# Kernel optimization log

Measured on AMD Instinct MI355X. Metric: run time of the kernel, lower is better.

## Reference

```python
import jax, jax.numpy as jnp
import numpy as np

WEIGHT = 0.1  # init weight

# 6-connectivity (scipy generate_binary_structure(3,1)) neighbor reductions

def _nmin(x, fill):
    p = jnp.pad(x, 1, constant_values=fill)
    return jnp.minimum(
        jnp.minimum(jnp.minimum(p[:-2, 1:-1, 1:-1], p[2:, 1:-1, 1:-1]),
                    jnp.minimum(p[1:-1, :-2, 1:-1], p[1:-1, 2:, 1:-1])),
        jnp.minimum(p[1:-1, 1:-1, :-2], p[1:-1, 1:-1, 2:]))


def _nor(x):
    p = jnp.pad(x, 1, constant_values=False)
    return (p[:-2, 1:-1, 1:-1] | p[2:, 1:-1, 1:-1] |
            p[1:-1, :-2, 1:-1] | p[1:-1, 2:, 1:-1] |
            p[1:-1, 1:-1, :-2] | p[1:-1, 1:-1, 2:])


def _nand(x):
    # border_value=0 in scipy.binary_erosion -> pad with False
    p = jnp.pad(x, 1, constant_values=False)
    return (p[:-2, 1:-1, 1:-1] & p[2:, 1:-1, 1:-1] &
            p[1:-1, :-2, 1:-1] & p[1:-1, 2:, 1:-1] &
            p[1:-1, 1:-1, :-2] & p[1:-1, 1:-1, 2:])


def _cc_count(mask):
    # connected-component count via min-label propagation (6-connectivity),
    # equivalent to scipy.ndimage.label(...)[1]
    n = mask.size
    idx = jnp.arange(n, dtype=jnp.int32).reshape(mask.shape)
    big = jnp.int32(n)
    lbl0 = jnp.where(mask, idx, big)

    def body(c):
        lbl, _ = c
        new = jnp.where(mask, jnp.minimum(lbl, _nmin(lbl, big)), big)
        return new, jnp.any(new != lbl)

    lbl, _ = jax.lax.while_loop(lambda c: c[1], body, (lbl0, jnp.bool_(True)))
    # roots: voxels whose label equals their own index
    return jnp.sum(mask & (lbl == idx)).astype(jnp.int32)


def _cavity_volume(mask):
    # binary_fill_holes: background not reachable from the border
    bg = ~mask
    border = jnp.ones(mask.shape, bool).at[1:-1, 1:-1, 1:-1].set(False)
    r0 = bg & border

    def body(c):
        r, _ = c
        new = bg & (r | _nor(r))
        return new, jnp.any(new != r)

    reach, _ = jax.lax.while_loop(lambda c: c[1], body, (r0, jnp.bool_(True)))
    return jnp.sum(bg & ~reach).astype(jnp.int32)


def _betti(mask):
    b0 = _cc_count(mask)
    eroded = mask & _nand(mask)  # binary_erosion, iterations=1
    b0e = _cc_count(eroded)
    b1 = jnp.maximum(jnp.int32(0), b0 - b0e)
    b2 = _cavity_volume(mask) // 100
    return jnp.stack([b0, b1, b2]).astype(jnp.float32)


def setup_inputs() -> dict:
    key = jax.random.key(0)
    k1, k2 = jax.random.split(key)
    B, C, D, H, W = 2, 4, 64, 128, 128
    pred = jax.random.normal(k1, (B, C, D, H, W), dtype=jnp.float32)
    target = jax.random.randint(k2, (B, D, H, W), 0, C, dtype=jnp.int32)
    return {"pred": pred, "target": target}


def reference(pred, target):
    B, C = pred.shape[0], pred.shape[1]
    vol = pred.shape[2:]
    prob = jax.nn.softmax(pred, axis=1)
    # foreground classes 1..C-1, flattened to [B*(C-1), D, H, W]
    pred_masks = (prob[:, 1:] > 0.5).reshape((-1,) + vol)
    cls = jnp.arange(1, C, dtype=target.dtype).reshape(1, C - 1, 1, 1, 1)
    tgt_masks = (target[:, None] == cls).reshape((-1,) + vol)
    pb = jax.vmap(_betti)(pred_masks)  # [B*(C-1), 3]
    tb = jax.vmap(_betti)(tgt_masks)
    count = B * (C - 1)
    return WEIGHT * jnp.abs(pb - tb).sum() / count
```

## Files before the change

### kernel.cpp

```cpp
#include <hip/hip_runtime.h>
#include <stdint.h>

#define DD 64
#define HH 128
#define WW 128
#define NVOX (DD * HH * WW)
#define NWRD (NVOX / 32)
#define BATCH 2
#define NCLS 4
#define NMASK 12
#define NSLOT 24
#define NTILE 128
#define MAXC 2048
#define VNODE (NTILE * MAXC)
#define NODE_STRIDE (VNODE + 64)
#define NTASKW 7424
#define NTASKH (2 * NTASKW)

__device__ __forceinline__ int uf_find(int* P, int x) {
    while (true) {
        int p = P[x];
        if (p == x) return x;
        int gp = P[p];
        if (gp != p) P[x] = gp;
        x = gp;
    }
}
__device__ __forceinline__ int uf_find_ro(const int* P, int x) {
    int p;
    while ((p = P[x]) != x) x = p;
    return x;
}
__device__ __forceinline__ int2 uf_find2_ro(const int* P, int a, int b) {
    while (true) {
        int pa = P[a];
        int pb = P[b];
        bool da = (pa == a), db = (pb == b);
        if (da && db) return make_int2(a, b);
        a = pa; b = pb;
    }
}
__device__ __forceinline__ void uf_union(int* P, int a, int b) {
    while (true) {
        a = uf_find(P, a);
        b = uf_find(P, b);
        if (a == b) return;
        int lo = a < b ? a : b;
        int hi = a < b ? b : a;
        int old = atomicCAS(&P[hi], hi, lo);
        if (old == hi) return;
        a = lo; b = old;
    }
}

#define SW(v) ((v) + ((v) >> 5))
__device__ __forceinline__ int lfind(int* lp, int x) {
    while (true) {
        int p = lp[SW(x)];
        if (p == x) return x;
        int gp = lp[SW(p)];
        if (gp != p) lp[SW(x)] = gp;
        x = gp;
    }
}
__device__ __forceinline__ void lunion(int* lp, int a, int b) {
    while (true) {
        a = lfind(lp, a);
        b = lfind(lp, b);
        if (a == b) return;
        int lo = a < b ? a : b;
        int hi = a < b ? b : a;
        int old = atomicCAS(&lp[SW(hi)], hi, lo);
        if (old == hi) return;
        a = lo; b = old;
    }
}
__device__ __forceinline__ int lresolve(const int* lp, int h) {
    int v = lp[SW(h)];
    while (v >= 0) v = lp[SW(v)];
    return -v - 1;
}
__device__ __forceinline__ int run_head(uint32_t w, int p) {
    uint32_t below = ~w & ((1u << p) - 1u);
    return below ? (32 - __clz((int)below)) : 0;
}


__global__ void k_masks2(const float* __restrict__ pred, const int* __restrict__ tgt,
                         uint32_t* __restrict__ maskW, int* __restrict__ counts) {
    int tid = blockIdx.x * blockDim.x + threadIdx.x;
    if (tid < 64) counts[tid] = 0;
    int b = tid >> 20;
    int i = tid & (NVOX - 1);
    const float* p = pred + (size_t)b * NCLS * NVOX + i;
    float x0 = p[0], x1 = p[NVOX], x2 = p[2 * NVOX], x3 = p[3 * NVOX];
    float mx = fmaxf(fmaxf(x0, x1), fmaxf(x2, x3));
    float e0 = __expf(x0 - mx), e1 = __expf(x1 - mx), e2 = __expf(x2 - mx), e3 = __expf(x3 - mx);
    float S = e0 + e1 + e2 + e3;
    int t = tgt[(size_t)b * NVOX + i];
    int lane = threadIdx.x & 63;
    int wbase = i >> 5;
    float ev[3] = {e1, e2, e3};
    for (int c = 0; c < 3; ++c) {
        unsigned long long bal = __ballot(ev[c] / S > 0.5f);
        uint32_t* M = maskW + (size_t)(b * 3 + c) * NWRD;
        if (lane == 0)  M[wbase] = (uint32_t)bal;
        if (lane == 32) M[wbase] = (uint32_t)(bal >> 32);
        unsigned long long balT = __ballot(t == c + 1);
        uint32_t* MT = maskW + (size_t)(6 + b * 3 + c) * NWRD;
        if (lane == 0)  MT[wbase] = (uint32_t)balT;
        if (lane == 32) MT[wbase] = (uint32_t)(balT >> 32);
    }
}

__global__ void k_erode(const uint32_t* __restrict__ maskW, uint32_t* __restrict__ erodW) {
    int tid = blockIdx.x * blockDim.x + threadIdx.x;
    int m = tid / NWRD;
    int w = tid - m * NWRD;
    const uint32_t* M = maskW + (size_t)m * NWRD;
    int z = w >> 9, y = (w >> 2) & 127, q = w & 3;
    uint32_t a = M[w];
    uint32_t xl = (a << 1) | (q ? (M[w - 1] >> 31) : 0u);
    uint32_t xr = (a >> 1) | (q < 3 ? (M[w + 1] << 31) : 0u);
    uint32_t ym = (y > 0)   ? M[w - 4]   : 0u;
    uint32_t yp = (y < 127) ? M[w + 4]   : 0u;
    uint32_t zm = (z > 0)   ? M[w - 512] : 0u;
    uint32_t zp = (z < 63)  ? M[w + 512] : 0u;
    erodW[tid] = a & xl & xr & ym & yp & zm & zp;
}

__global__ void k_local(const uint32_t* __restrict__ maskW, const uint32_t* __restrict__ erodW,
                        uint16_t* __restrict__ C16all, int* __restrict__ Pall,
                        uint16_t* __restrict__ volAll, int* __restrict__ tcount, int m0) {
    __shared__ int lp[8448];
    __shared__ uint32_t aw[256];
    __shared__ uint32_t lvol[MAXC / 2];
    __shared__ int lcount;
    int slot = blockIdx.y;
    int pr = m0 + slot;
    bool comb = pr < 12;
    int m = comb ? pr : pr - 12;
    uint16_t* C16 = C16all + (size_t)slot * NVOX;
    int* P = Pall + (size_t)slot * NODE_STRIDE;
    int tile = blockIdx.x;
    int tz = tile >> 4, ty = tile & 15;
    int t2 = threadIdx.x;
    int lane = t2 & 63;
    int wl = t2 >> 1;
    int h  = t2 & 1;
    int zl = wl >> 5, yl = (wl >> 2) & 7, q = wl & 3;
    int gw = ((tz * 8 + zl) * 128 + (ty * 8 + yl)) * 4 + q;
    uint32_t afull = comb ? maskW[m * NWRD + gw] : erodW[m * NWRD + gw];
    if (h == 0) aw[wl] = afull;
    uint32_t a16 = (afull >> (16 * h)) & 0xFFFFu;
    uint32_t av = ~a16 & 0xFFFFu;
    if (t2 == 0) lcount = 0;
    if (comb && tile == 0 && t2 == 0) P[VNODE] = VNODE;

    if (!comb) {
        int any = __syncthreads_count(a16 != 0);
        if (any == 0) {
            if (t2 == 0) tcount[slot * NTILE + tile] = 0;
            return;
        }
    }

    int lbase = t2 << 4;
    uint32_t heads = comb ? (((a16 ^ (a16 << 1)) | 1u) & 0xFFFFu)
                          : (a16 & ~(a16 << 1) & 0xFFFFu);
    {
        uint32_t st = heads;
        while (st) { int p = __ffs(st) - 1; st &= st - 1; lp[SW(lbase + p)] = lbase + p; }
    }
    __syncthreads();

    if (comb) {
        {
            int v0 = a16 & 1;
            if (h == 1) {
                uint32_t lo = afull & 0xFFFFu;
                if ((int)((lo >> 15) & 1) == v0) {
                    uint32_t pm = v0 ? lo : (~lo & 0xFFFFu);
                    lunion(lp, lbase, lbase - 16 + run_head(pm, 15));
                }
            } else if (q) {
                uint32_t hi = aw[wl - 1] >> 16;
                if ((int)((hi >> 15) & 1) == v0) {
                    uint32_t pm = v0 ? hi : (~hi & 0xFFFFu);
                    lunion(lp, lbase, lbase - 16 + run_head(pm, 15));
                }
            }
        }
        if (yl < 7) {
            uint32_t nb = (aw[wl + 4] >> (16 * h)) & 0xFFFFu;
            uint32_t nv = ~nb & 0xFFFFu;
            uint32_t ov = a16 & nb;
            uint32_t st = ov & ~(ov << 1);
            int la = -1, lb = -1;
            while (st) {
                int p = __ffs(st) - 1; st &= st - 1;
                int ha = lbase + run_head(a16, p);
                int hb = lbase + 128 + run_head(nb, p);
                if (ha != la || hb != lb) { lunion(lp, ha, hb); la = ha; lb = hb; }
            }
            ov = av & nv;
            st = ov & ~(ov << 1);
            la = -1; lb = -1;
            while (st) {
                int p = __ffs(st) - 1; st &= st - 1;
                int ha = lbase + run_head(av, p);
                int hb = lbase + 128 + run_head(nv, p);
                if (ha != la || hb != lb) { lunion(lp, ha, hb); la = ha; lb = hb; }
            }
        }
        if (zl < 7) {
            uint32_t nb = (aw[wl + 32] >> (16 * h)) & 0xFFFFu;
            uint32_t nv = ~nb & 0xFFFFu;
            uint32_t ov = a16 & nb;
            uint32_t st = ov & ~(ov << 1);
            int la = -1, lb = -1;
            while (st) {
                int p = __ffs(st) - 1; st &= st - 1;
                int ha = lbase + run_head(a16, p);
                int hb = lbase + 1024 + run_head(nb, p);
                if (ha != la || hb != lb) { lunion(lp, ha, hb); la = ha; lb = hb; }
            }
            ov = av & nv;
            st = ov & ~(ov << 1);
            la = -1; lb = -1;
            while (st) {
                int p = __ffs(st) - 1; st &= st - 1;
                int ha = lbase + run_head(av, p);
                int hb = lbase + 1024 + run_head(nv, p);
                if (ha != la || hb != lb) { lunion(lp, ha, hb); la = ha; lb = hb; }
            }
        }
    } else if (a16) {
        if (a16 & 1u) {
            if (h == 1) {
                uint32_t lo16 = afull & 0xFFFFu;
                if (lo16 >> 15) lunion(lp, lbase, lbase - 16 + run_head(lo16, 15));
            } else if (q) {
                uint32_t hi16 = aw[wl - 1] >> 16;
                if (hi16 >> 15) lunion(lp, lbase, lbase - 16 + run_head(hi16, 15));
            }
        }
        if (yl < 7) {
            uint32_t by = (aw[wl + 4] >> (16 * h)) & 0xFFFFu;
            uint32_t ov = a16 & by;
            uint32_t st = ov & ~(ov << 1);
            int la = -1, lb = -1;
            while (st) {
                int p = __ffs(st) - 1; st &= st - 1;
                int ha = lbase + run_head(a16, p);
                int hb = lbase + 128 + run_head(by, p);
                if (ha != la || hb != lb) { lunion(lp, ha, hb); la = ha; lb = hb; }
            }
        }
        if (zl < 7) {
            uint32_t bz = (aw[wl + 32] >> (16 * h)) & 0xFFFFu;
            uint32_t ov = a16 & bz;
            uint32_t st = ov & ~(ov << 1);
            int la = -1, lb = -1;
            while (st) {
                int p = __ffs(st) - 1; st &= st - 1;
                int ha = lbase + run_head(a16, p);
                int hb = lbase + 1024 + run_head(bz, p);
                if (ha != la || hb != lb) { lunion(lp, ha, hb); la = ha; lb = hb; }
            }
        }
    }
    __syncthreads();

    if (comb) { lvol[t2] = 0; lvol[t2 + 512] = 0; }

    int tileBase = tile * MAXC;
    {
        uint32_t rootMask = 0; int nrF = 0, nrB = 0;
        uint32_t st = heads;
        while (st) {
            int p = __ffs(st) - 1; st &= st - 1;
            int hh = lbase + p;
            if (lp[SW(hh)] == hh) {
                rootMask |= 1u << p;
                if (comb && !((a16 >> p) & 1)) ++nrB; else ++nrF;
            }
        }
        int packed = nrF | (nrB << 16);
        int pre = packed;
        for (int off = 1; off < 64; off <<= 1) {
            int v = __shfl_up(pre, off);
            if (lane >= off) pre += v;
        }
        int waveTot = __shfl(pre, 63);
        int base = 0;
        if (lane == 63 && waveTot) base = atomicAdd(&lcount, waveTot);
        base = __shfl(base, 63);
        int excl = pre - packed;
        int kF = (base & 0xFFFF) + (excl & 0xFFFF);
        int kB = ((unsigned)base >> 16) + ((unsigned)excl >> 16);
        st = rootMask;
        while (st) {
            int p = __ffs(st) - 1; st &= st - 1;
            int hh = lbase + p;
            int id;
            if (!comb || ((a16 >> p) & 1)) id = kF++;
            else                           id = MAXC - 1 - (kB++);
            lp[SW(hh)] = -id - 1;
            P[tileBase + id] = tileBase + id;
        }
    }
    __syncthreads();

    if (t2 == 0) tcount[slot * NTILE + tile] = lcount;

    int myId = -1, myLen = 0; bool multi = false;
    bool faceRow = (yl == 0 || yl == 7 || zl == 0 || zl == 7);
    if (comb || (a16 && faceRow)) {
        int i0 = (gw << 5) + 16 * h;
        int gz = tz * 8 + zl, gy = ty * 8 + yl;
        bool bordRow = comb && (gz == 0 || gz == 63 || gy == 0 || gy == 127);
        bool uniHalf = (a16 == 0xFFFFu) || (comb && a16 == 0);
        if (faceRow && uniHalf) {
            int id = lresolve(lp, lbase);
            uint32_t pk = (uint32_t)id * 0x10001u;
            uint4 v4 = make_uint4(pk, pk, pk, pk);
            uint4* dst = (uint4*)(C16 + i0);
            dst[0] = v4; dst[1] = v4;
            if (comb && a16 == 0) {
                myId = id; myLen = 16;
                if (bordRow || (q == 0 && h == 0) || (q == 3 && h == 1))
                    P[tileBase + id] = VNODE;
            }
        } else if (faceRow) {
            uint32_t wv[8] = {0, 0, 0, 0, 0, 0, 0, 0};
            int id = 0;
            bool xs = (q == 0 && h == 0), xe = (q == 3 && h == 1);
            #pragma unroll
            for (int j = 0; j < 16; ++j) {
                bool bg = comb && !((a16 >> j) & 1);
                if ((heads >> j) & 1) {
                    id = lresolve(lp, lbase + j);
                    if (bg) {
                        if (myLen == 0) myId = id;
                        else if (id != myId) multi = true;
                        if (bordRow || (xs && j == 0)) P[tileBase + id] = VNODE;
                    }
                }
                if (bg) {
                    ++myLen;
                    if (xe && j == 15) P[tileBase + id] = VNODE;
                }
                wv[j >> 1] |= ((uint32_t)(uint16_t)id) << ((j & 1) * 16);
            }
            uint4* dst = (uint4*)(C16 + i0);
            dst[0] = make_uint4(wv[0], wv[1], wv[2], wv[3]);
            dst[1] = make_uint4(wv[4], wv[5], wv[6], wv[7]);
        } else {
            uint32_t it = heads & av;
            int htopB = (!((a16 >> 15) & 1)) ? run_head(av, 15) : -1;
            while (it) {
                int p = __ffs(it) - 1; it &= it - 1;
                int id = lresolve(lp, lbase + p);
                uint32_t run = av >> p;
                int len = __ffs(~run) - 1;
                if (myLen == 0) myId = id;
                else if (id != myId) multi = true;
                myLen += len;
                if ((q == 0 && h == 0 && p == 0) || (q == 3 && h == 1 && p == htopB))
                    P[tileBase + id] = VNODE;
            }
        }
    }

    if (comb) {
        unsigned long long hasMask = __ballot(myLen > 0);
        if (hasMask) {
            bool anyMulti = __any(multi);
            int firstLane = __ffsll(hasMask) - 1;
            int leadId = __shfl(myId, firstLane);
            bool uni = !anyMulti && __all(myLen == 0 || myId == leadId);
            if (uni) {
                int s = myLen;
                for (int off = 32; off; off >>= 1) s += __shfl_down(s, off);
                if (lane == 0 && s)
                    atomicAdd(&lvol[leadId >> 1], (uint32_t)s << ((leadId & 1) * 16));
            } else if (myLen > 0) {
                if (!multi) {
                    atomicAdd(&lvol[myId >> 1], (uint32_t)myLen << ((myId & 1) * 16));
                } else {
                    uint32_t st = heads & av;
                    while (st) {
                        int p = __ffs(st) - 1; st &= st - 1;
                        int id = lresolve(lp, lbase + p);
                        uint32_t run = av >> p;
                        int len = __ffs(~run) - 1;
                        atomicAdd(&lvol[id >> 1], (uint32_t)len << ((id & 1) * 16));
                    }
                }
            }
        }
    }
    __syncthreads();

    if (comb) {
        int lcB = lcount >> 16;
        uint16_t* volC = volAll + (size_t)slot * (NTILE * MAXC) + tileBase;
        for (int k = t2; k < lcB; k += 512) {
            int idx = MAXC - 1 - k;
            volC[idx] = (uint16_t)((lvol[idx >> 1] >> ((idx & 1) * 16)) & 0xFFFFu);
        }
    }
}

__global__ void k_bmerge(const uint32_t* __restrict__ maskW, const uint32_t* __restrict__ erodW,
                         const uint16_t* __restrict__ C16all, int* __restrict__ Pall,
                         int m0) {
    int slot = blockIdx.y;
    int pr = m0 + slot;
    bool comb = pr < 12;
    int m = comb ? pr : pr - 12;
    int pass = blockIdx.z;
    if (!comb && pass) return;

    int t = blockIdx.x * blockDim.x + threadIdx.x;
    bool act = (t < NTASKH);
    int wt = t >> 1, h = t & 1;

    int w = 0, dw = 4, dv = WW, tA = 0, tB = 0;
    if (act) {
        if (wt < 3840) {
            int q = wt & 3, r = wt >> 2;
            int yi = r >> 6, z = r & 63;
            int y = 8 * yi + 7;
            w = (z * 128 + y) * 4 + q;
            dw = 4; dv = WW;
            tA = ((z >> 3) * 16 + yi) * MAXC;
            tB = tA + MAXC;
        } else {
            int tt = wt - 3840;
            int q = tt & 3, r = tt >> 2;
            int zi = r >> 7, y = r & 127;
            int z = 8 * zi + 7;
            w = (z * 128 + y) * 4 + q;
            dw = 512; dv = HH * WW;
            tA = (zi * 16 + (y >> 3)) * MAXC;
            tB = tA + 16 * MAXC;
        }
    }

    uint32_t st = 0;
    if (act) {
        uint32_t a, b = 0;
        if (comb) {
            a = maskW[m * NWRD + w];
            b = maskW[m * NWRD + w + dw];
        } else {
            a = erodW[m * NWRD + w];
            if ((a >> (16 * h)) & 0xFFFFu) b = erodW[m * NWRD + w + dw];
        }
        uint32_t ah = (a >> (16 * h)) & 0xFFFFu;
        uint32_t bh = (b >> (16 * h)) & 0xFFFFu;
        if (pass) { ah = ~ah & 0xFFFFu; bh = ~bh & 0xFFFFu; }
        uint32_t ov = ah & bh;
        st = ov & ~(ov << 1);
    }

    const uint16_t* C16 = C16all + (size_t)slot * NVOX;
    int* P = Pall + (size_t)slot * NODE_STRIDE;
    int i0 = (w << 5) + 16 * h;

    int ca = -1, cb = -1, p0 = -1;
    if (st) {
        p0 = __ffs(st) - 1;
        ca = tA + C16[i0 + p0];
        cb = tB + C16[i0 + p0 + dv];
    }
    int la = __shfl_up(ca, 1);
    int lb = __shfl_up(cb, 1);
    if ((threadIdx.x & 63) == 0) { la = -1; lb = -1; }

    while (st) {
        int p = __ffs(st) - 1; st &= st - 1;
        int xa, xb;
        if (p == p0) { xa = ca; xb = cb; }
        else { xa = tA + C16[i0 + p]; xb = tB + C16[i0 + p + dv]; }
        if (xa != la || xb != lb) { uf_union(P, xa, xb); la = xa; lb = xb; }
    }
}

__global__ void k_flatc(const int* __restrict__ Pall, const uint16_t* __restrict__ volAll,
                        const int* __restrict__ tcount, int* __restrict__ counts, int m0) {
    __shared__ int sAcc;
    __shared__ int sRootV;
    int slot = blockIdx.y;
    int pr = m0 + slot;
    bool comb = pr < 12;
    int m = comb ? pr : pr - 12;
    int tile = blockIdx.x;
    const int* P = Pall + (size_t)slot * NODE_STRIDE;
    int tc = tcount[slot * NTILE + tile];
    int lcF = tc & 0xFFFF, lcB = (unsigned)tc >> 16;
    if (threadIdx.x == 0) {
        sAcc = 0;
        sRootV = comb ? uf_find_ro(P, VNODE) : 0;
    }
    __syncthreads();
    int tileBase = tile * MAXC;
    int bd = blockDim.x;
    int cnt = 0;
    for (int k = threadIdx.x; k < lcF; k += 2 * bd) {
        int k2 = k + bd;
        if (k2 < lcF) {
            int2 r = uf_find2_ro(P, tileBase + k, tileBase + k2);
            cnt += (r.x == tileBase + k) + (r.y == tileBase + k2);
        } else {
            if (uf_find_ro(P, tileBase + k) == tileBase + k) ++cnt;
        }
    }
    if (comb && lcB) {
        const uint16_t* volC = volAll + (size_t)slot * (NTILE * MAXC) + tileBase;
        int rootV = sRootV;
        for (int k = threadIdx.x; k < lcB; k += 2 * bd) {
            int k2 = k + bd;
            int i1 = MAXC - 1 - k;
            if (k2 < lcB) {
                int i2 = MAXC - 1 - k2;
                int2 r = uf_find2_ro(P, tileBase + i1, tileBase + i2);
                if (r.x != rootV) cnt += (int)volC[i1] << 16;
                if (r.y != rootV) cnt += (int)volC[i2] << 16;
            } else {
                if (uf_find_ro(P, tileBase + i1) != rootV) cnt += (int)volC[i1] << 16;
            }
        }
    }
    for (int off = 32; off; off >>= 1) cnt += __shfl_down(cnt, off);
    if ((threadIdx.x & 63) == 0 && cnt) atomicAdd(&sAcc, cnt);
    __syncthreads();
    if (threadIdx.x == 0 && sAcc) {
        int f = sAcc & 0xFFFF;
        int v = (unsigned)sAcc >> 16;
        if (comb) {
            if (f) atomicAdd(&counts[m], f);
            if (v) atomicAdd(&counts[24 + m], v);
        } else if (f) {
            atomicAdd(&counts[12 + m], f);
        }
    }
}

__global__ void k_loss(const int* __restrict__ counts, float* __restrict__ out) {
    if (threadIdx.x != 0 || blockIdx.x != 0) return;
    float acc = 0.f;
    for (int m = 0; m < 6; ++m) {
        int pb0 = counts[m],      pbe = counts[12 + m],      pcv = counts[24 + m];
        int tb0 = counts[6 + m],  tbe = counts[12 + 6 + m],  tcv = counts[24 + 6 + m];
        int pb1 = max(0, pb0 - pbe), tb1 = max(0, tb0 - tbe);
        int pb2 = pcv / 100, tb2 = tcv / 100;
        acc += fabsf((float)(pb0 - tb0)) + fabsf((float)(pb1 - tb1)) + fabsf((float)(pb2 - tb2));
    }
    out[0] = 0.1f * acc / 6.0f;
}

extern "C" void kernel_launch(void* const* d_in, const int* in_sizes, int n_in,
                              void* d_out, int out_size, void* d_ws, size_t ws_size,
                              hipStream_t stream) {
    const float* pred = (const float*)d_in[0];
    const int* tgt = (const int*)d_in[1];
    float* out = (float*)d_out;

    uint8_t* ws = (uint8_t*)d_ws;
    uint32_t* maskW = (uint32_t*)ws;
    size_t off = (size_t)NMASK * NWRD * 4;
    uint32_t* erodW = (uint32_t*)(ws + off);
    off += (size_t)NMASK * NWRD * 4;
    int* counts = (int*)(ws + off);
    off += 256;
    int* tcount = (int*)(ws + off);
    off += (size_t)NSLOT * NTILE * 4;
    off = (off + 255) & ~(size_t)255;

    size_t avail = ws_size > off ? ws_size - off : 0;
    size_t slot_bytes = (size_t)NVOX * 2 + (size_t)NODE_STRIDE * 4
                      + (size_t)NTILE * MAXC * 2;
    int PB = (int)(avail / slot_bytes);
    if (PB > NSLOT) PB = NSLOT;
    if (PB < 1) PB = 1;

    uint16_t* C16all = (uint16_t*)(ws + off);
    int* Pall = (int*)(ws + off + (size_t)PB * NVOX * 2);
    uint16_t* volAll = (uint16_t*)(ws + off + (size_t)PB * NVOX * 2
                                   + (size_t)PB * NODE_STRIDE * 4);

    k_masks2<<<dim3((BATCH * NVOX) / 256), 256, 0, stream>>>(pred, tgt, maskW, counts);
    k_erode<<<dim3((NMASK * NWRD) / 256), 256, 0, stream>>>(maskW, erodW);

    for (int m0 = 0; m0 < NSLOT; m0 += PB) {
        int mb = PB < (NSLOT - m0) ? PB : (NSLOT - m0);
        k_local <<<dim3(NTILE, mb), 512, 0, stream>>>(maskW, erodW, C16all, Pall,
                                                      volAll, tcount, m0);
        k_bmerge<<<dim3((NTASKH + 255) / 256, mb, 2), 256, 0, stream>>>(maskW, erodW,
                                                                        C16all, Pall, m0);
        k_flatc <<<dim3(NTILE, mb), 256, 0, stream>>>(Pall, volAll, tcount, counts, m0);
    }

    k_loss<<<1, 64, 0, stream>>>(counts, out);
}
```

Baseline: 212.7 us.

## Restructure slot batching: split combined k_local launches, single bmerge/flatc pass

When the workspace holds all 24 slots, the host now launches k_local in several smaller grids (four launches of 3 combined masks, then one of 12 eroded masks), followed by one k_bmerge and one k_flatc over all slots. Slot indexing is decoupled from blockIdx via an sbase parameter, and tcount is indexed by the global slot. The per-run-head label initialisation in shared memory is replaced by an unconditional unrolled fill of all 16 entries per thread. The intent is to balance heavy combined-mask tiles against cheap eroded ones and cut launch count for the merge and count phases, at the cost of extra k_local launches.

After: 287.8 us. 35.3% more time.

```diff
diff --git a/kernel.cpp b/kernel.cpp
--- a/kernel.cpp
+++ b/kernel.cpp
@@ -131,17 +131,18 @@
 
 __global__ void k_local(const uint32_t* __restrict__ maskW, const uint32_t* __restrict__ erodW,
                         uint16_t* __restrict__ C16all, int* __restrict__ Pall,
-                        uint16_t* __restrict__ volAll, int* __restrict__ tcount, int m0) {
+                        uint16_t* __restrict__ volAll, int* __restrict__ tcount,
+                        int m0, int sbase) {
     __shared__ int lp[8448];
     __shared__ uint32_t aw[256];
     __shared__ uint32_t lvol[MAXC / 2];
     __shared__ int lcount;
-    int slot = blockIdx.y;
-    int pr = m0 + slot;
+    int pr = m0 + blockIdx.y;
+    int sslot = pr - sbase;
     bool comb = pr < 12;
     int m = comb ? pr : pr - 12;
-    uint16_t* C16 = C16all + (size_t)slot * NVOX;
-    int* P = Pall + (size_t)slot * NODE_STRIDE;
+    uint16_t* C16 = C16all + (size_t)sslot * NVOX;
+    int* P = Pall + (size_t)sslot * NODE_STRIDE;
     int tile = blockIdx.x;
     int tz = tile >> 4, ty = tile & 15;
     int t2 = threadIdx.x;
@@ -160,7 +161,7 @@
     if (!comb) {
         int any = __syncthreads_count(a16 != 0);
         if (any == 0) {
-            if (t2 == 0) tcount[slot * NTILE + tile] = 0;
+            if (t2 == 0) tcount[pr * NTILE + tile] = 0;
             return;
         }
     }
@@ -168,10 +169,8 @@
     int lbase = t2 << 4;
     uint32_t heads = comb ? (((a16 ^ (a16 << 1)) | 1u) & 0xFFFFu)
                           : (a16 & ~(a16 << 1) & 0xFFFFu);
-    {
-        uint32_t st = heads;
-        while (st) { int p = __ffs(st) - 1; st &= st - 1; lp[SW(lbase + p)] = lbase + p; }
-    }
+    #pragma unroll
+    for (int j = 0; j < 16; ++j) lp[SW(lbase + j)] = lbase + j;
     __syncthreads();
 
     if (comb) {
@@ -312,7 +311,7 @@
     }
     __syncthreads();
 
-    if (t2 == 0) tcount[slot * NTILE + tile] = lcount;
+    if (t2 == 0) tcount[pr * NTILE + tile] = lcount;
 
     int myId = -1, myLen = 0; bool multi = false;
     bool faceRow = (yl == 0 || yl == 7 || zl == 0 || zl == 7);
@@ -405,7 +404,7 @@
 
     if (comb) {
         int lcB = lcount >> 16;
-        uint16_t* volC = volAll + (size_t)slot * (NTILE * MAXC) + tileBase;
+        uint16_t* volC = volAll + (size_t)sslot * (NTILE * MAXC) + tileBase;
         for (int k = t2; k < lcB; k += 512) {
             int idx = MAXC - 1 - k;
             volC[idx] = (uint16_t)((lvol[idx >> 1] >> ((idx & 1) * 16)) & 0xFFFFu);
@@ -415,9 +414,9 @@
 
 __global__ void k_bmerge(const uint32_t* __restrict__ maskW, const uint32_t* __restrict__ erodW,
                          const uint16_t* __restrict__ C16all, int* __restrict__ Pall,
-                         int m0) {
-    int slot = blockIdx.y;
-    int pr = m0 + slot;
+                         int m0, int sbase) {
+    int pr = m0 + blockIdx.y;
+    int sslot = pr - sbase;
     bool comb = pr < 12;
     int m = comb ? pr : pr - 12;
     int pass = blockIdx.z;
@@ -466,8 +465,8 @@
         st = ov & ~(ov << 1);
     }
 
-    const uint16_t* C16 = C16all + (size_t)slot * NVOX;
-    int* P = Pall + (size_t)slot * NODE_STRIDE;
+    const uint16_t* C16 = C16all + (size_t)sslot * NVOX;
+    int* P = Pall + (size_t)sslot * NODE_STRIDE;
     int i0 = (w << 5) + 16 * h;
 
     int ca = -1, cb = -1, p0 = -1;
@@ -490,16 +489,17 @@
 }
 
 __global__ void k_flatc(const int* __restrict__ Pall, const uint16_t* __restrict__ volAll,
-                        const int* __restrict__ tcount, int* __restrict__ counts, int m0) {
+                        const int* __restrict__ tcount, int* __restrict__ counts,
+                        int m0, int sbase) {
     __shared__ int sAcc;
     __shared__ int sRootV;
-    int slot = blockIdx.y;
-    int pr = m0 + slot;
+    int pr = m0 + blockIdx.y;
+    int sslot = pr - sbase;
     bool comb = pr < 12;
     int m = comb ? pr : pr - 12;
     int tile = blockIdx.x;
-    const int* P = Pall + (size_t)slot * NODE_STRIDE;
-    int tc = tcount[slot * NTILE + tile];
+    const int* P = Pall + (size_t)sslot * NODE_STRIDE;
+    int tc = tcount[pr * NTILE + tile];
     int lcF = tc & 0xFFFF, lcB = (unsigned)tc >> 16;
     if (threadIdx.x == 0) {
         sAcc = 0;
@@ -519,7 +519,7 @@
         }
     }
     if (comb && lcB) {
-        const uint16_t* volC = volAll + (size_t)slot * (NTILE * MAXC) + tileBase;
+        const uint16_t* volC = volAll + (size_t)sslot * (NTILE * MAXC) + tileBase;
         int rootV = sRootV;
         for (int k = threadIdx.x; k < lcB; k += 2 * bd) {
             int k2 = k + bd;
@@ -595,13 +595,26 @@
     k_masks2<<<dim3((BATCH * NVOX) / 256), 256, 0, stream>>>(pred, tgt, maskW, counts);
     k_erode<<<dim3((NMASK * NWRD) / 256), 256, 0, stream>>>(maskW, erodW);
 
-    for (int m0 = 0; m0 < NSLOT; m0 += PB) {
-        int mb = PB < (NSLOT - m0) ? PB : (NSLOT - m0);
-        k_local <<<dim3(NTILE, mb), 512, 0, stream>>>(maskW, erodW, C16all, Pall,
-                                                      volAll, tcount, m0);
-        k_bmerge<<<dim3((NTASKH + 255) / 256, mb, 2), 256, 0, stream>>>(maskW, erodW,
-                                                                        C16all, Pall, m0);
-        k_flatc <<<dim3(NTILE, mb), 256, 0, stream>>>(Pall, volAll, tcount, counts, m0);
+    if (PB >= NSLOT) {
+        for (int m0 = 0; m0 < 12; m0 += 3)
+            k_local<<<dim3(NTILE, 3), 512, 0, stream>>>(maskW, erodW, C16all, Pall,
+                                                        volAll, tcount, m0, 0);
+        k_local<<<dim3(NTILE, 12), 512, 0, stream>>>(maskW, erodW, C16all, Pall,
+                                                     volAll, tcount, 12, 0);
+        k_bmerge<<<dim3((NTASKH + 255) / 256, NSLOT, 2), 256, 0, stream>>>(
+            maskW, erodW, C16all, Pall, 0, 0);
+        k_flatc<<<dim3(NTILE, NSLOT), 256, 0, stream>>>(Pall, volAll, tcount, counts, 0, 0);
+    } else {
+        for (int m0 = 0; m0 < NSLOT; m0 += PB) {
+            int mb = PB < (NSLOT - m0) ? PB : (NSLOT - m0);
+            k_local <<<dim3(NTILE, mb), 512, 0, stream>>>(maskW, erodW, C16all, Pall,
+                                                          volAll, tcount, m0, m0);
+            k_bmerge<<<dim3((NTASKH + 255) / 256, mb, 2), 256, 0, stream>>>(maskW, erodW,
+                                                                            C16all, Pall,
+                                                                            m0, m0);
+            k_flatc <<<dim3(NTILE, mb), 256, 0, stream>>>(Pall, volAll, tcount, counts,
+                                                          m0, m0);
+        }
     }
 
     k_loss<<<1, 64, 0, stream>>>(counts, out);
```
